# Performance work log

Measured on AMD Instinct MI355X. Metric: run time of the kernel, lower is better.

The kernel has to match this reference:

```python
import jax, jax.numpy as jnp
import numpy as np

N_NODES = 50000
N_EDGES = 800000
F_IN = 128
HIDDEN = 32
HEADS = 4
F_OUT = 64
NEG_SLOPE = 0.2


def setup_inputs() -> dict:
    key = jax.random.key(0)
    ks = jax.random.split(key, 9)
    x = jax.random.normal(ks[0], (N_NODES, F_IN), dtype=jnp.float32)
    edge_index = jax.random.randint(ks[1], (2, N_EDGES), 0, N_NODES, dtype=jnp.int64)
    edge_weight = jax.random.uniform(ks[2], (N_EDGES,), dtype=jnp.float32)
    # GATConv parameters
    W = jax.random.normal(ks[3], (F_IN, HEADS * HIDDEN), dtype=jnp.float32) * (1.0 / np.sqrt(F_IN))
    a_src = jax.random.normal(ks[4], (HEADS, HIDDEN), dtype=jnp.float32) * 0.1
    a_dst = jax.random.normal(ks[5], (HEADS, HIDDEN), dtype=jnp.float32) * 0.1
    bias = jnp.zeros((HEADS * HIDDEN,), dtype=jnp.float32)
    # output linear
    W2 = jax.random.normal(ks[6], (HEADS * HIDDEN, F_OUT), dtype=jnp.float32) * (1.0 / np.sqrt(HEADS * HIDDEN))
    b2 = jnp.zeros((F_OUT,), dtype=jnp.float32)
    return {"x": x, "edge_index": edge_index, "edge_weight": edge_weight,
            "W": W, "a_src": a_src, "a_dst": a_dst, "bias": bias,
            "W2": W2, "b2": b2}


def reference(x, edge_index, edge_weight, W, a_src, a_dst, bias, W2, b2):
    src, dst = edge_index[0], edge_index[1]
    # linear transform per head: [N, H, C]
    h = (x @ W).reshape(-1, HEADS, HIDDEN)
    # per-node attention logits: [N, H]
    alpha_s = jnp.einsum('nhc,hc->nh', h, a_src)
    alpha_d = jnp.einsum('nhc,hc->nh', h, a_dst)
    # per-edge scores: [E, H]
    e = alpha_s[src] + alpha_d[dst]
    e = jnp.where(e >= 0, e, NEG_SLOPE * e)  # LeakyReLU(0.2)
    # segment softmax over destination neighborhoods
    m = jax.ops.segment_max(e, dst, num_segments=N_NODES)  # [N, H]
    ex = jnp.exp(e - m[dst])
    denom = jax.ops.segment_sum(ex, dst, num_segments=N_NODES)  # [N, H]
    alpha = ex / (denom[dst] + 1e-16)  # [E, H]
    # weighted scatter-add aggregation: [N, H, C]
    msgs = alpha[:, :, None] * h[src]
    out = jax.ops.segment_sum(msgs, dst, num_segments=N_NODES)
    out = out.reshape(-1, HEADS * HIDDEN) + bias
    out = jax.nn.elu(out)
    return out @ W2 + b2
```

## Files before the change

kernel.cpp:

```cpp
#include <hip/hip_runtime.h>

#define N_NODES 50000
#define N_EDGES 800000
#define F_IN 128
#define HH 128
#define HEADS 4
#define HIDDEN 32
#define F_OUT 64
#define NEG_SLOPE 0.2f
#define CAP 64

#define NODE_BLOCKS ((N_NODES + 31) / 32)
#define FILL_BLOCKS ((N_EDGES / 4 + 255) / 256)
#define ZERO_BLOCKS ((N_NODES + 255) / 256)

typedef __attribute__((ext_vector_type(8))) short short8v;
typedef __attribute__((ext_vector_type(4))) float float4v;

__device__ __forceinline__ unsigned short f2bf(float f) {
    unsigned int u = __float_as_uint(f);
    u = (u + 0x7FFFu + ((u >> 16) & 1u)) >> 16;
    return (unsigned short)u;
}
__device__ __forceinline__ float bf2f(unsigned short s) {
    return __uint_as_float((unsigned int)s << 16);
}

__global__ __launch_bounds__(256) void k_prep(
    const float* __restrict__ W, const float* __restrict__ a_src,
    const float* __restrict__ a_dst,
    unsigned short* __restrict__ Wf, unsigned short* __restrict__ Waf,
    int* __restrict__ cursor)
{
    const int b = blockIdx.x;
    const int t = threadIdx.x;

    if (b >= 9) {
        int i = (b - 9) * 256 + t;
        if (i < N_NODES) cursor[i] = 0;
        return;
    }

    if (b < 8) {
        const int ks = b >> 1, nn = b & 1;
        const int w = t >> 6, lane = t & 63, l15 = lane & 15, l4 = lane >> 4;
        const int c  = w * 32 + nn * 16 + l15;
        const int kb = ks * 32 + l4 * 8;
        short8v frag;
        #pragma unroll
        for (int j = 0; j < 8; ++j)
            frag[j] = (short)f2bf(W[(size_t)(kb + j) * HH + c]);
        *(short8v*)&Wf[(size_t)((ks * 2 + nn) * 256 + t) * 8] = frag;
        return;
    }

    __shared__ float Wa[F_IN][8];
    #pragma unroll
    for (int i = 0; i < 4; ++i) {
        int idx = t * 4 + i;
        int k = idx >> 3, col = idx & 7;
        const float* av = (col < 4) ? a_src : a_dst;
        int hd = col & 3;
        float s = 0.f;
        #pragma unroll
        for (int cc = 0; cc < 32; ++cc)
            s = fmaf(W[(size_t)k * HH + hd * 32 + cc], av[hd * 32 + cc], s);
        Wa[k][col] = s;
    }
    __syncthreads();

    if (t < 64) {
        const int l15 = t & 15, l4 = t >> 4;
        #pragma unroll
        for (int ks = 0; ks < 4; ++ks) {
            short8v frag;
            #pragma unroll
            for (int j = 0; j < 8; ++j)
                frag[j] = (l15 < 8) ? (short)f2bf(Wa[ks * 32 + l4 * 8 + j][l15]) : (short)0;
            *(short8v*)&Waf[(size_t)(ks * 64 + t) * 8] = frag;
        }
    }
}

__global__ __launch_bounds__(256) void k_node_fill(
    const float* __restrict__ x,
    const unsigned short* __restrict__ Wf, const unsigned short* __restrict__ Waf,
    unsigned short* __restrict__ h_bf,
    float* __restrict__ as_out, float* __restrict__ ad_out,
    const int* __restrict__ ei, int* __restrict__ cursor, int* __restrict__ bucket)
{
    __shared__ __align__(16) unsigned short xs[32][136];

    if (blockIdx.x >= NODE_BLOCKS) {
        int e0 = ((blockIdx.x - NODE_BLOCKS) * 256 + threadIdx.x) * 4;
        if (e0 < N_EDGES) {
            int4 s4 = *(const int4*)&ei[e0];
            int4 d4 = *(const int4*)&ei[N_EDGES + e0];
            bucket[(size_t)d4.x * CAP + (atomicAdd(&cursor[d4.x], 1) & (CAP - 1))] = s4.x;
            bucket[(size_t)d4.y * CAP + (atomicAdd(&cursor[d4.y], 1) & (CAP - 1))] = s4.y;
            bucket[(size_t)d4.z * CAP + (atomicAdd(&cursor[d4.z], 1) & (CAP - 1))] = s4.z;
            bucket[(size_t)d4.w * CAP + (atomicAdd(&cursor[d4.w], 1) & (CAP - 1))] = s4.w;
        }
        return;
    }

    const int tid  = threadIdx.x;
    const int base = blockIdx.x * 32;

    for (int i = tid; i < 32 * 32; i += 256) {
        int r = i >> 5, c4 = i & 31;
        int n = base + r;
        float4 v = (n < N_NODES) ? *(const float4*)&x[(size_t)n * F_IN + c4 * 4]
                                 : make_float4(0.f, 0.f, 0.f, 0.f);
        ushort4 hv;
        hv.x = f2bf(v.x); hv.y = f2bf(v.y); hv.z = f2bf(v.z); hv.w = f2bf(v.w);
        *(ushort4*)&xs[r][c4 * 4] = hv;
    }
    __syncthreads();

    const int w    = tid >> 6;
    const int lane = tid & 63;
    const int l15  = lane & 15;
    const int l4   = lane >> 4;

    short8v bfrag[4][2], wafrag[4];
    #pragma unroll
    for (int ks = 0; ks < 4; ++ks) {
        bfrag[ks][0] = *(const short8v*)&Wf[(size_t)((ks * 2 + 0) * 256 + tid) * 8];
        bfrag[ks][1] = *(const short8v*)&Wf[(size_t)((ks * 2 + 1) * 256 + tid) * 8];
        wafrag[ks]   = *(const short8v*)&Waf[(size_t)(ks * 64 + lane) * 8];
    }

    float4v acc[2][2] = {};
    float4v accL[2] = {};
    #pragma unroll
    for (int ks = 0; ks < 4; ++ks) {
        short8v a0 = *(const short8v*)&xs[l15][ks * 32 + l4 * 8];
        short8v a1 = *(const short8v*)&xs[16 + l15][ks * 32 + l4 * 8];
        acc[0][0] = __builtin_amdgcn_mfma_f32_16x16x32_bf16(a0, bfrag[ks][0], acc[0][0], 0, 0, 0);
        acc[0][1] = __builtin_amdgcn_mfma_f32_16x16x32_bf16(a0, bfrag[ks][1], acc[0][1], 0, 0, 0);
        acc[1][0] = __builtin_amdgcn_mfma_f32_16x16x32_bf16(a1, bfrag[ks][0], acc[1][0], 0, 0, 0);
        acc[1][1] = __builtin_amdgcn_mfma_f32_16x16x32_bf16(a1, bfrag[ks][1], acc[1][1], 0, 0, 0);
        accL[0]   = __builtin_amdgcn_mfma_f32_16x16x32_bf16(a0, wafrag[ks], accL[0], 0, 0, 0);
        accL[1]   = __builtin_amdgcn_mfma_f32_16x16x32_bf16(a1, wafrag[ks], accL[1], 0, 0, 0);
    }

    if (w == 0 && l15 < 8) {
        #pragma unroll
        for (int m = 0; m < 2; ++m) {
            #pragma unroll
            for (int reg = 0; reg < 4; ++reg) {
                int node = base + m * 16 + l4 * 4 + reg;
                if (node >= N_NODES) continue;
                float lg = accL[m][reg];
                if (l15 < 4) as_out[node * HEADS + l15]       = lg;
                else         ad_out[node * HEADS + (l15 - 4)] = lg;
            }
        }
    }

    __syncthreads();
    #pragma unroll
    for (int m = 0; m < 2; ++m) {
        #pragma unroll
        for (int reg = 0; reg < 4; ++reg) {
            int r = m * 16 + l4 * 4 + reg;
            xs[r][w * 32 + l15]      = f2bf(acc[m][0][reg]);
            xs[r][w * 32 + 16 + l15] = f2bf(acc[m][1][reg]);
        }
    }
    __syncthreads();
    for (int i = tid; i < 32 * 16; i += 256) {
        int r = i >> 4, c8 = i & 15;
        int n = base + r;
        if (n < N_NODES)
            *(short8v*)&h_bf[(size_t)n * HH + c8 * 8] = *(const short8v*)&xs[r][c8 * 8];
    }
}

__global__ __launch_bounds__(256) void k_gather(
    const int* __restrict__ cnt_arr, const int* __restrict__ bucket,
    const float* __restrict__ as_, const float* __restrict__ ad_,
    const unsigned short* __restrict__ h_bf, unsigned short* __restrict__ agg_bf)
{
    int gid = blockIdx.x * 256 + threadIdx.x;
    int n = gid >> 6;
    if (n >= N_NODES) return;
    const int lane = gid & 63;
    const int hd  = lane >> 4;
    const int e16 = lane & 15;

    const float advv = ad_[n * 4 + hd];
    const int cnt = cnt_arr[n];
    const int* brow = &bucket[(size_t)n * CAP];

    float accx = 0.f, accy = 0.f, sum = 0.f;

    for (int cb = 0; cb < cnt; cb += 16) {
        int m = cnt - cb; if (m > 16) m = 16;
        int s = 0; float exown = 0.f;
        if (e16 < m) {
            s = brow[cb + e16];
            float lg = as_[s * 4 + hd] + advv;
            lg = lg >= 0.f ? lg : NEG_SLOPE * lg;
            exown = __expf(lg);
        }

#define GAT_BODY(j)                                                            \
        {                                                                      \
            float al = __shfl(exown, (hd << 4) + (j));                         \
            int   sj = __shfl(s,     (hd << 4) + (j));                         \
            unsigned int hv = *(const unsigned int*)&h_bf[(size_t)sj * HH + lane * 2]; \
            sum += al;                                                         \
            accx = fmaf(al, __uint_as_float((hv & 0xFFFFu) << 16), accx);      \
            accy = fmaf(al, __uint_as_float(hv & 0xFFFF0000u), accy);          \
        }

        if (m == 16) {
            #pragma unroll
            for (int j = 0; j < 16; ++j) GAT_BODY(j)
        } else {
            for (int j = 0; j < m; ++j) GAT_BODY(j)
        }
#undef GAT_BODY
    }

    float inv = 1.f / (sum + 1e-16f);
    unsigned int packed = (unsigned int)f2bf(accx * inv)
                        | ((unsigned int)f2bf(accy * inv) << 16);
    *(unsigned int*)&agg_bf[(size_t)n * HH + lane * 2] = packed;
}

__global__ __launch_bounds__(256) void k_output(
    const unsigned short* __restrict__ agg_bf, const float* __restrict__ bias,
    const float* __restrict__ W2, const float* __restrict__ b2,
    float* __restrict__ out)
{
    __shared__ float eb[64][132];

    const int tid  = threadIdx.x;
    const int base = blockIdx.x * 64;

    for (int i = tid; i < 64 * 16; i += 256) {
        int r = i >> 4, c8 = i & 15;
        int n = base + r;
        float v[8];
        if (n < N_NODES) {
            ushort4 p0 = *(const ushort4*)&agg_bf[(size_t)n * HH + c8 * 8];
            ushort4 p1 = *(const ushort4*)&agg_bf[(size_t)n * HH + c8 * 8 + 4];
            v[0] = bf2f(p0.x); v[1] = bf2f(p0.y); v[2] = bf2f(p0.z); v[3] = bf2f(p0.w);
            v[4] = bf2f(p1.x); v[5] = bf2f(p1.y); v[6] = bf2f(p1.z); v[7] = bf2f(p1.w);
        } else {
            #pragma unroll
            for (int j = 0; j < 8; ++j) v[j] = 0.f;
        }
        #pragma unroll
        for (int j = 0; j < 8; ++j) {
            float t = v[j] + bias[c8 * 8 + j];
            eb[r][c8 * 8 + j] = t > 0.f ? t : __expf(t) - 1.f;
        }
    }
    __syncthreads();

    const int cg = tid & 15;
    const int q  = tid >> 4;

    float4 b2v = *(const float4*)&b2[cg * 4];
    float4 acc[4] = { b2v, b2v, b2v, b2v };
    for (int k4 = 0; k4 < 32; ++k4) {
        const float* wr = &W2[(k4 * 4) * F_OUT + cg * 4];
        float4 w0 = *(const float4*)(wr);
        float4 w1 = *(const float4*)(wr + F_OUT);
        float4 w2 = *(const float4*)(wr + 2 * F_OUT);
        float4 w3 = *(const float4*)(wr + 3 * F_OUT);
        #pragma unroll
        for (int j = 0; j < 4; ++j) {
            float4 xv = *(const float4*)&eb[q * 4 + j][k4 * 4];
            acc[j].x = fmaf(xv.x, w0.x, acc[j].x); acc[j].y = fmaf(xv.x, w0.y, acc[j].y);
            acc[j].z = fmaf(xv.x, w0.z, acc[j].z); acc[j].w = fmaf(xv.x, w0.w, acc[j].w);
            acc[j].x = fmaf(xv.y, w1.x, acc[j].x); acc[j].y = fmaf(xv.y, w1.y, acc[j].y);
            acc[j].z = fmaf(xv.y, w1.z, acc[j].z); acc[j].w = fmaf(xv.y, w1.w, acc[j].w);
            acc[j].x = fmaf(xv.z, w2.x, acc[j].x); acc[j].y = fmaf(xv.z, w2.y, acc[j].y);
            acc[j].z = fmaf(xv.z, w2.z, acc[j].z); acc[j].w = fmaf(xv.z, w2.w, acc[j].w);
            acc[j].x = fmaf(xv.w, w3.x, acc[j].x); acc[j].y = fmaf(xv.w, w3.y, acc[j].y);
            acc[j].z = fmaf(xv.w, w3.z, acc[j].z); acc[j].w = fmaf(xv.w, w3.w, acc[j].w);
        }
    }
    #pragma unroll
    for (int j = 0; j < 4; ++j) {
        int n = base + q * 4 + j;
        if (n < N_NODES)
            *(float4*)&out[(size_t)n * F_OUT + cg * 4] = acc[j];
    }
}

extern "C" void kernel_launch(void* const* d_in, const int* in_sizes, int n_in,
                              void* d_out, int out_size, void* d_ws, size_t ws_size,
                              hipStream_t stream)
{
    const float* x     = (const float*)d_in[0];
    const int*   ei    = (const int*)  d_in[1];
    const float* W     = (const float*)d_in[3];
    const float* a_src = (const float*)d_in[4];
    const float* a_dst = (const float*)d_in[5];
    const float* bias  = (const float*)d_in[6];
    const float* W2    = (const float*)d_in[7];
    const float* b2    = (const float*)d_in[8];
    float* out = (float*)d_out;

    char* ws = (char*)d_ws;
    unsigned short* Wf   = (unsigned short*)ws;
    unsigned short* Waf  = Wf + 8 * 256 * 8;
    unsigned short* h_bf = Waf + 4 * 64 * 8;
    float* as_   = (float*)(h_bf + (size_t)N_NODES * HH);
    float* ad_   = as_ + (size_t)N_NODES * HEADS;
    int*   cursor= (int*)(ad_ + (size_t)N_NODES * HEADS);
    int*   bucket= cursor + N_NODES;
    unsigned short* agg_bf = (unsigned short*)(bucket + (size_t)N_NODES * CAP);

    k_prep<<<9 + ZERO_BLOCKS, 256, 0, stream>>>(W, a_src, a_dst, Wf, Waf, cursor);
    k_node_fill<<<NODE_BLOCKS + FILL_BLOCKS, 256, 0, stream>>>(
        x, Wf, Waf, h_bf, as_, ad_, ei, cursor, bucket);
    k_gather<<<(N_NODES * 64 + 255) / 256, 256, 0, stream>>>(cursor, bucket, as_, ad_, h_bf, agg_bf);
    k_output<<<(N_NODES + 63) / 64, 256, 0, stream>>>(agg_bf, bias, W2, b2, out);
}
```

Baseline: 124.9 us.

## Bin edges per 64-node group and fuse gather with output projection

```diff
diff --git a/kernel.cpp b/kernel.cpp
--- a/kernel.cpp
+++ b/kernel.cpp
@@ -5,14 +5,17 @@
 #define F_IN 128
 #define HH 128
 #define HEADS 4
-#define HIDDEN 32
 #define F_OUT 64
 #define NEG_SLOPE 0.2f
-#define CAP 64
+
+#define NBIN ((N_NODES + 63) / 64)
+#define XC 8
+#define CAPXB 256
+#define NCUR (NBIN * XC)
 
 #define NODE_BLOCKS ((N_NODES + 31) / 32)
 #define FILL_BLOCKS ((N_EDGES / 4 + 255) / 256)
-#define ZERO_BLOCKS ((N_NODES + 255) / 256)
+#define ZERO_BLOCKS ((NCUR + 255) / 256)
 
 typedef __attribute__((ext_vector_type(8))) short short8v;
 typedef __attribute__((ext_vector_type(4))) float float4v;
@@ -21,9 +24,6 @@
     unsigned int u = __float_as_uint(f);
     u = (u + 0x7FFFu + ((u >> 16) & 1u)) >> 16;
     return (unsigned short)u;
-}
-__device__ __forceinline__ float bf2f(unsigned short s) {
-    return __uint_as_float((unsigned int)s << 16);
 }
 
 __global__ __launch_bounds__(256) void k_prep(
@@ -37,7 +37,7 @@
 
     if (b >= 9) {
         int i = (b - 9) * 256 + t;
-        if (i < N_NODES) cursor[i] = 0;
+        if (i < NCUR) cursor[i] = 0;
         return;
     }
 
@@ -87,19 +87,27 @@
     const unsigned short* __restrict__ Wf, const unsigned short* __restrict__ Waf,
     unsigned short* __restrict__ h_bf,
     float* __restrict__ as_out, float* __restrict__ ad_out,
-    const int* __restrict__ ei, int* __restrict__ cursor, int* __restrict__ bucket)
+    const int* __restrict__ ei, int* __restrict__ cursor, unsigned int* __restrict__ bins)
 {
     __shared__ __align__(16) unsigned short xs[32][136];
 
     if (blockIdx.x >= NODE_BLOCKS) {
+        const int vx = blockIdx.x & 7;
         int e0 = ((blockIdx.x - NODE_BLOCKS) * 256 + threadIdx.x) * 4;
         if (e0 < N_EDGES) {
             int4 s4 = *(const int4*)&ei[e0];
             int4 d4 = *(const int4*)&ei[N_EDGES + e0];
-            bucket[(size_t)d4.x * CAP + (atomicAdd(&cursor[d4.x], 1) & (CAP - 1))] = s4.x;
-            bucket[(size_t)d4.y * CAP + (atomicAdd(&cursor[d4.y], 1) & (CAP - 1))] = s4.y;
-            bucket[(size_t)d4.z * CAP + (atomicAdd(&cursor[d4.z], 1) & (CAP - 1))] = s4.z;
-            bucket[(size_t)d4.w * CAP + (atomicAdd(&cursor[d4.w], 1) & (CAP - 1))] = s4.w;
+            #define PUTEDGE(S, D)                                              \
+            {                                                                  \
+                int idx = ((D) >> 6) * XC + vx;                                \
+                int sl = atomicAdd(&cursor[idx], 1);                           \
+                if (sl < CAPXB)                                                \
+                    bins[(size_t)idx * CAPXB + sl] =                           \
+                        ((unsigned int)(S) << 6) | (unsigned int)((D) & 63);   \
+            }
+            PUTEDGE(s4.x, d4.x) PUTEDGE(s4.y, d4.y)
+            PUTEDGE(s4.z, d4.z) PUTEDGE(s4.w, d4.w)
+            #undef PUTEDGE
         }
         return;
     }
@@ -178,95 +186,115 @@
     }
 }
 
-__global__ __launch_bounds__(256) void k_gather(
-    const int* __restrict__ cnt_arr, const int* __restrict__ bucket,
+__global__ __launch_bounds__(256) void k_gather_out(
+    const int* __restrict__ cursor, const unsigned int* __restrict__ bins,
     const float* __restrict__ as_, const float* __restrict__ ad_,
-    const unsigned short* __restrict__ h_bf, unsigned short* __restrict__ agg_bf)
+    const unsigned short* __restrict__ h_bf,
+    const float* __restrict__ bias, const float* __restrict__ W2,
+    const float* __restrict__ b2, float* __restrict__ out)
 {
-    int gid = blockIdx.x * 256 + threadIdx.x;
-    int n = gid >> 6;
-    if (n >= N_NODES) return;
-    const int lane = gid & 63;
-    const int hd  = lane >> 4;
-    const int e16 = lane & 15;
-
-    const float advv = ad_[n * 4 + hd];
-    const int cnt = cnt_arr[n];
-    const int* brow = &bucket[(size_t)n * CAP];
-
-    float accx = 0.f, accy = 0.f, sum = 0.f;
-
-    for (int cb = 0; cb < cnt; cb += 16) {
-        int m = cnt - cb; if (m > 16) m = 16;
-        int s = 0; float exown = 0.f;
-        if (e16 < m) {
-            s = brow[cb + e16];
-            float lg = as_[s * 4 + hd] + advv;
-            lg = lg >= 0.f ? lg : NEG_SLOPE * lg;
-            exown = __expf(lg);
-        }
+    __shared__ unsigned int stg[XC * CAPXB];
+    __shared__ unsigned short srcs[XC * CAPXB];
+    __shared__ int lcnt[64], loff[64], lcur[64];
+    __shared__ int scnt[XC], soff[XC], tot_s;
+    __shared__ float eb[64][132];
+    __shared__ float biasl[HH];
+
+    const int bin = blockIdx.x;
+    const int tid = threadIdx.x;
+
+    if (tid < 64) { lcnt[tid] = 0; lcur[tid] = 0; }
+    if (tid < HH) biasl[tid] = bias[tid];
+    if (tid < XC) {
+        int c = cursor[bin * XC + tid];
+        scnt[tid] = c < CAPXB ? c : CAPXB;
+    }
+    __syncthreads();
+    if (tid == 0) {
+        int r = 0;
+        #pragma unroll
+        for (int j = 0; j < XC; ++j) { soff[j] = r; r += scnt[j]; }
+        tot_s = r;
+    }
+    __syncthreads();
+    #pragma unroll
+    for (int sg = 0; sg < XC; ++sg) {
+        int c = scnt[sg], o = soff[sg];
+        const unsigned int* bp = &bins[(size_t)(bin * XC + sg) * CAPXB];
+        for (int i = tid; i < c; i += 256) {
+            unsigned int u = bp[i];
+            stg[o + i] = u;
+            atomicAdd(&lcnt[u & 63], 1);
+        }
+    }
+    __syncthreads();
+    if (tid == 0) {
+        int r = 0;
+        #pragma unroll
+        for (int j = 0; j < 64; ++j) { loff[j] = r; r += lcnt[j]; }
+    }
+    __syncthreads();
+    const int tot = tot_s;
+    for (int i = tid; i < tot; i += 256) {
+        unsigned int u = stg[i];
+        int d = u & 63;
+        int sl = loff[d] + atomicAdd(&lcur[d], 1);
+        srcs[sl] = (unsigned short)(u >> 6);
+    }
+    __syncthreads();
+
+    const int wv   = tid >> 6;
+    const int lane = tid & 63;
+    const int hd   = lane >> 4;
+    const int e16  = lane & 15;
+
+    for (int i = 0; i < 16; ++i) {
+        int ln = wv * 16 + i;
+        int n = bin * 64 + ln;
+        if (n >= N_NODES) continue;
+        const int deg = lcnt[ln], off = loff[ln];
+        const float advv = ad_[n * 4 + hd];
+
+        float accx = 0.f, accy = 0.f, sum = 0.f;
+        for (int cb = 0; cb < deg; cb += 16) {
+            int m = deg - cb; if (m > 16) m = 16;
+            int s = 0; float exown = 0.f;
+            if (e16 < m) {
+                s = srcs[off + cb + e16];
+                float lg = as_[s * 4 + hd] + advv;
+                lg = lg >= 0.f ? lg : NEG_SLOPE * lg;
+                exown = __expf(lg);
+            }
 
 #define GAT_BODY(j)                                                            \
-        {                                                                      \
-            float al = __shfl(exown, (hd << 4) + (j));                         \
-            int   sj = __shfl(s,     (hd << 4) + (j));                         \
-            unsigned int hv = *(const unsigned int*)&h_bf[(size_t)sj * HH + lane * 2]; \
-            sum += al;                                                         \
-            accx = fmaf(al, __uint_as_float((hv & 0xFFFFu) << 16), accx);      \
-            accy = fmaf(al, __uint_as_float(hv & 0xFFFF0000u), accy);          \
-        }
-
-        if (m == 16) {
-            #pragma unroll
-            for (int j = 0; j < 16; ++j) GAT_BODY(j)
-        } else {
-            for (int j = 0; j < m; ++j) GAT_BODY(j)
-        }
+            {                                                                  \
+                float al = __shfl(exown, (hd << 4) + (j));                     \
+                int   sj = __shfl(s,     (hd << 4) + (j));                     \
+                unsigned int hv = *(const unsigned int*)&h_bf[(size_t)sj * HH + lane * 2]; \
+                sum += al;                                                     \
+                accx = fmaf(al, __uint_as_float((hv & 0xFFFFu) << 16), accx);  \
+                accy = fmaf(al, __uint_as_float(hv & 0xFFFF0000u), accy);      \
+            }
+            if (m == 16) {
+                #pragma unroll
+                for (int j = 0; j < 16; ++j) GAT_BODY(j)
+            } else {
+                for (int j = 0; j < m; ++j) GAT_BODY(j)
+            }
 #undef GAT_BODY
-    }
-
-    float inv = 1.f / (sum + 1e-16f);
-    unsigned int packed = (unsigned int)f2bf(accx * inv)
-                        | ((unsigned int)f2bf(accy * inv) << 16);
-    *(unsigned int*)&agg_bf[(size_t)n * HH + lane * 2] = packed;
-}
-
-__global__ __launch_bounds__(256) void k_output(
-    const unsigned short* __restrict__ agg_bf, const float* __restrict__ bias,
-    const float* __restrict__ W2, const float* __restrict__ b2,
-    float* __restrict__ out)
-{
-    __shared__ float eb[64][132];
-
-    const int tid  = threadIdx.x;
-    const int base = blockIdx.x * 64;
-
-    for (int i = tid; i < 64 * 16; i += 256) {
-        int r = i >> 4, c8 = i & 15;
-        int n = base + r;
-        float v[8];
-        if (n < N_NODES) {
-            ushort4 p0 = *(const ushort4*)&agg_bf[(size_t)n * HH + c8 * 8];
-            ushort4 p1 = *(const ushort4*)&agg_bf[(size_t)n * HH + c8 * 8 + 4];
-            v[0] = bf2f(p0.x); v[1] = bf2f(p0.y); v[2] = bf2f(p0.z); v[3] = bf2f(p0.w);
-            v[4] = bf2f(p1.x); v[5] = bf2f(p1.y); v[6] = bf2f(p1.z); v[7] = bf2f(p1.w);
-        } else {
-            #pragma unroll
-            for (int j = 0; j < 8; ++j) v[j] = 0.f;
-        }
-        #pragma unroll
-        for (int j = 0; j < 8; ++j) {
-            float t = v[j] + bias[c8 * 8 + j];
-            eb[r][c8 * 8 + j] = t > 0.f ? t : __expf(t) - 1.f;
-        }
+        }
+        float inv = 1.f / (sum + 1e-16f);
+        float v0 = accx * inv + biasl[lane * 2];
+        float v1 = accy * inv + biasl[lane * 2 + 1];
+        eb[ln][lane * 2]     = v0 > 0.f ? v0 : __expf(v0) - 1.f;
+        eb[ln][lane * 2 + 1] = v1 > 0.f ? v1 : __expf(v1) - 1.f;
     }
     __syncthreads();
 
     const int cg = tid & 15;
     const int q  = tid >> 4;
-
     float4 b2v = *(const float4*)&b2[cg * 4];
-    float4 acc[4] = { b2v, b2v, b2v, b2v };
+    float4 oacc[4] = { b2v, b2v, b2v, b2v };
     for (int k4 = 0; k4 < 32; ++k4) {
         const float* wr = &W2[(k4 * 4) * F_OUT + cg * 4];
         float4 w0 = *(const float4*)(wr);
@@ -276,21 +304,21 @@
         #pragma unroll
         for (int j = 0; j < 4; ++j) {
             float4 xv = *(const float4*)&eb[q * 4 + j][k4 * 4];
-            acc[j].x = fmaf(xv.x, w0.x, acc[j].x); acc[j].y = fmaf(xv.x, w0.y, acc[j].y);
-            acc[j].z = fmaf(xv.x, w0.z, acc[j].z); acc[j].w = fmaf(xv.x, w0.w, acc[j].w);
-            acc[j].x = fmaf(xv.y, w1.x, acc[j].x); acc[j].y = fmaf(xv.y, w1.y, acc[j].y);
-            acc[j].z = fmaf(xv.y, w1.z, acc[j].z); acc[j].w = fmaf(xv.y, w1.w, acc[j].w);
-            acc[j].x = fmaf(xv.z, w2.x, acc[j].x); acc[j].y = fmaf(xv.z, w2.y, acc[j].y);
-            acc[j].z = fmaf(xv.z, w2.z, acc[j].z); acc[j].w = fmaf(xv.z, w2.w, acc[j].w);
-            acc[j].x = fmaf(xv.w, w3.x, acc[j].x); acc[j].y = fmaf(xv.w, w3.y, acc[j].y);
-            acc[j].z = fmaf(xv.w, w3.z, acc[j].z); acc[j].w = fmaf(xv.w, w3.w, acc[j].w);
+            oacc[j].x = fmaf(xv.x, w0.x, oacc[j].x); oacc[j].y = fmaf(xv.x, w0.y, oacc[j].y);
+            oacc[j].z = fmaf(xv.x, w0.z, oacc[j].z); oacc[j].w = fmaf(xv.x, w0.w, oacc[j].w);
+            oacc[j].x = fmaf(xv.y, w1.x, oacc[j].x); oacc[j].y = fmaf(xv.y, w1.y, oacc[j].y);
+            oacc[j].z = fmaf(xv.y, w1.z, oacc[j].z); oacc[j].w = fmaf(xv.y, w1.w, oacc[j].w);
+            oacc[j].x = fmaf(xv.z, w2.x, oacc[j].x); oacc[j].y = fmaf(xv.z, w2.y, oacc[j].y);
+            oacc[j].z = fmaf(xv.z, w2.z, oacc[j].z); oacc[j].w = fmaf(xv.z, w2.w, oacc[j].w);
+            oacc[j].x = fmaf(xv.w, w3.x, oacc[j].x); oacc[j].y = fmaf(xv.w, w3.y, oacc[j].y);
+            oacc[j].z = fmaf(xv.w, w3.z, oacc[j].z); oacc[j].w = fmaf(xv.w, w3.w, oacc[j].w);
         }
     }
     #pragma unroll
     for (int j = 0; j < 4; ++j) {
-        int n = base + q * 4 + j;
+        int n = bin * 64 + q * 4 + j;
         if (n < N_NODES)
-            *(float4*)&out[(size_t)n * F_OUT + cg * 4] = acc[j];
+            *(float4*)&out[(size_t)n * F_OUT + cg * 4] = oacc[j];
     }
 }
 
@@ -315,12 +343,11 @@
     float* as_   = (float*)(h_bf + (size_t)N_NODES * HH);
     float* ad_   = as_ + (size_t)N_NODES * HEADS;
     int*   cursor= (int*)(ad_ + (size_t)N_NODES * HEADS);
-    int*   bucket= cursor + N_NODES;
-    unsigned short* agg_bf = (unsigned short*)(bucket + (size_t)N_NODES * CAP);
+    unsigned int* bins = (unsigned int*)(cursor + 6400);
 
     k_prep<<<9 + ZERO_BLOCKS, 256, 0, stream>>>(W, a_src, a_dst, Wf, Waf, cursor);
     k_node_fill<<<NODE_BLOCKS + FILL_BLOCKS, 256, 0, stream>>>(
-        x, Wf, Waf, h_bf, as_, ad_, ei, cursor, bucket);
-    k_gather<<<(N_NODES * 64 + 255) / 256, 256, 0, stream>>>(cursor, bucket, as_, ad_, h_bf, agg_bf);
-    k_output<<<(N_NODES + 63) / 64, 256, 0, stream>>>(agg_bf, bias, W2, b2, out);
-}
+        x, Wf, Waf, h_bf, as_, ad_, ei, cursor, bins);
+    k_gather_out<<<NBIN, 256, 0, stream>>>(
+        cursor, bins, as_, ad_, h_bf, bias, W2, b2, out);
+}
```

Measured after the change: 202.8 us. +62.3%, slower.

## Bin edges by 64-node groups then counting-sort into compact CSR

Applied to the files above, without the earlier changes.

```diff
diff --git a/kernel.cpp b/kernel.cpp
--- a/kernel.cpp
+++ b/kernel.cpp
@@ -5,14 +5,18 @@
 #define F_IN 128
 #define HH 128
 #define HEADS 4
-#define HIDDEN 32
 #define F_OUT 64
 #define NEG_SLOPE 0.2f
-#define CAP 64
+
+#define NBIN ((N_NODES + 63) / 64)
+#define XC 8
+#define CAPXB 256
+#define NCUR (NBIN * XC)
+#define BINCAP (XC * CAPXB)
 
 #define NODE_BLOCKS ((N_NODES + 31) / 32)
 #define FILL_BLOCKS ((N_EDGES / 4 + 255) / 256)
-#define ZERO_BLOCKS ((N_NODES + 255) / 256)
+#define ZERO_BLOCKS ((NCUR + 255) / 256)
 
 typedef __attribute__((ext_vector_type(8))) short short8v;
 typedef __attribute__((ext_vector_type(4))) float float4v;
@@ -37,7 +41,7 @@
 
     if (b >= 9) {
         int i = (b - 9) * 256 + t;
-        if (i < N_NODES) cursor[i] = 0;
+        if (i < NCUR) cursor[i] = 0;
         return;
     }
 
@@ -87,19 +91,27 @@
     const unsigned short* __restrict__ Wf, const unsigned short* __restrict__ Waf,
     unsigned short* __restrict__ h_bf,
     float* __restrict__ as_out, float* __restrict__ ad_out,
-    const int* __restrict__ ei, int* __restrict__ cursor, int* __restrict__ bucket)
+    const int* __restrict__ ei, int* __restrict__ cursor, unsigned int* __restrict__ bins)
 {
     __shared__ __align__(16) unsigned short xs[32][136];
 
     if (blockIdx.x >= NODE_BLOCKS) {
+        const int vx = blockIdx.x & 7;
         int e0 = ((blockIdx.x - NODE_BLOCKS) * 256 + threadIdx.x) * 4;
         if (e0 < N_EDGES) {
             int4 s4 = *(const int4*)&ei[e0];
             int4 d4 = *(const int4*)&ei[N_EDGES + e0];
-            bucket[(size_t)d4.x * CAP + (atomicAdd(&cursor[d4.x], 1) & (CAP - 1))] = s4.x;
-            bucket[(size_t)d4.y * CAP + (atomicAdd(&cursor[d4.y], 1) & (CAP - 1))] = s4.y;
-            bucket[(size_t)d4.z * CAP + (atomicAdd(&cursor[d4.z], 1) & (CAP - 1))] = s4.z;
-            bucket[(size_t)d4.w * CAP + (atomicAdd(&cursor[d4.w], 1) & (CAP - 1))] = s4.w;
+            #define PUTEDGE(S, D)                                              \
+            {                                                                  \
+                int idx = ((D) >> 6) * XC + vx;                                \
+                int sl = atomicAdd(&cursor[idx], 1);                           \
+                if (sl < CAPXB)                                                \
+                    bins[(size_t)idx * CAPXB + sl] =                           \
+                        ((unsigned int)(S) << 6) | (unsigned int)((D) & 63);   \
+            }
+            PUTEDGE(s4.x, d4.x) PUTEDGE(s4.y, d4.y)
+            PUTEDGE(s4.z, d4.z) PUTEDGE(s4.w, d4.w)
+            #undef PUTEDGE
         }
         return;
     }
@@ -178,8 +190,63 @@
     }
 }
 
+__global__ __launch_bounds__(256) void k_sort(
+    const int* __restrict__ cursor, const unsigned int* __restrict__ bins,
+    unsigned short* __restrict__ srcs_g, int2* __restrict__ offdeg)
+{
+    __shared__ unsigned int stg[BINCAP];
+    __shared__ int lcnt[64], loff[64], lcur[64];
+    __shared__ int scnt[XC], soff[XC], tot_s;
+
+    const int bin = blockIdx.x;
+    const int tid = threadIdx.x;
+
+    if (tid < 64) { lcnt[tid] = 0; lcur[tid] = 0; }
+    if (tid < XC) {
+        int c = cursor[bin * XC + tid];
+        scnt[tid] = c < CAPXB ? c : CAPXB;
+    }
+    __syncthreads();
+    if (tid == 0) {
+        int r = 0;
+        #pragma unroll
+        for (int j = 0; j < XC; ++j) { soff[j] = r; r += scnt[j]; }
+        tot_s = r;
+    }
+    __syncthreads();
+    #pragma unroll
+    for (int sg = 0; sg < XC; ++sg) {
+        int c = scnt[sg], o = soff[sg];
+        const unsigned int* bp = &bins[(size_t)(bin * XC + sg) * CAPXB];
+        for (int i = tid; i < c; i += 256) {
+            unsigned int u = bp[i];
+            stg[o + i] = u;
+            atomicAdd(&lcnt[u & 63], 1);
+        }
+    }
+    __syncthreads();
+    if (tid == 0) {
+        int r = 0;
+        #pragma unroll
+        for (int j = 0; j < 64; ++j) { loff[j] = r; r += lcnt[j]; }
+    }
+    __syncthreads();
+    const int tot = tot_s;
+    for (int i = tid; i < tot; i += 256) {
+        unsigned int u = stg[i];
+        int d = u & 63;
+        int sl = loff[d] + atomicAdd(&lcur[d], 1);
+        srcs_g[(size_t)bin * BINCAP + sl] = (unsigned short)(u >> 6);
+    }
+    if (tid < 64) {
+        int n = bin * 64 + tid;
+        if (n < N_NODES)
+            offdeg[n] = make_int2(bin * BINCAP + loff[tid], lcnt[tid]);
+    }
+}
+
 __global__ __launch_bounds__(256) void k_gather(
-    const int* __restrict__ cnt_arr, const int* __restrict__ bucket,
+    const int2* __restrict__ offdeg, const unsigned short* __restrict__ srcs_g,
     const float* __restrict__ as_, const float* __restrict__ ad_,
     const unsigned short* __restrict__ h_bf, unsigned short* __restrict__ agg_bf)
 {
@@ -191,13 +258,14 @@
     const int e16 = lane & 15;
 
     const float advv = ad_[n * 4 + hd];
-    const int cnt = cnt_arr[n];
-    const int* brow = &bucket[(size_t)n * CAP];
+    const int2 od = offdeg[n];
+    const unsigned short* brow = &srcs_g[od.x];
+    const int deg = od.y;
 
     float accx = 0.f, accy = 0.f, sum = 0.f;
 
-    for (int cb = 0; cb < cnt; cb += 16) {
-        int m = cnt - cb; if (m > 16) m = 16;
+    for (int cb = 0; cb < deg; cb += 16) {
+        int m = deg - cb; if (m > 16) m = 16;
         int s = 0; float exown = 0.f;
         if (e16 < m) {
             s = brow[cb + e16];
@@ -315,12 +383,16 @@
     float* as_   = (float*)(h_bf + (size_t)N_NODES * HH);
     float* ad_   = as_ + (size_t)N_NODES * HEADS;
     int*   cursor= (int*)(ad_ + (size_t)N_NODES * HEADS);
-    int*   bucket= cursor + N_NODES;
-    unsigned short* agg_bf = (unsigned short*)(bucket + (size_t)N_NODES * CAP);
+    unsigned int* bins = (unsigned int*)(cursor + 6400);
+    unsigned short* srcs_g = (unsigned short*)(bins + (size_t)NBIN * BINCAP);
+    int2*  offdeg = (int2*)(srcs_g + (size_t)NBIN * BINCAP);
+    unsigned short* agg_bf = (unsigned short*)(offdeg + N_NODES + 2);
 
     k_prep<<<9 + ZERO_BLOCKS, 256, 0, stream>>>(W, a_src, a_dst, Wf, Waf, cursor);
     k_node_fill<<<NODE_BLOCKS + FILL_BLOCKS, 256, 0, stream>>>(
-        x, Wf, Waf, h_bf, as_, ad_, ei, cursor, bucket);
-    k_gather<<<(N_NODES * 64 + 255) / 256, 256, 0, stream>>>(cursor, bucket, as_, ad_, h_bf, agg_bf);
+        x, Wf, Waf, h_bf, as_, ad_, ei, cursor, bins);
+    k_sort<<<NBIN, 256, 0, stream>>>(cursor, bins, srcs_g, offdeg);
+    k_gather<<<(N_NODES * 64 + 255) / 256, 256, 0, stream>>>(
+        offdeg, srcs_g, as_, ad_, h_bf, agg_bf);
     k_output<<<(N_NODES + 63) / 64, 256, 0, stream>>>(agg_bf, bias, W2, b2, out);
 }
```

Measured after the change: 132.3 us. 5.9% more time.

## Store neighbor lists as 16-bit indices and interleave fill with node blocks

Applied to the files above, without the earlier changes.

```diff
diff --git a/kernel.cpp b/kernel.cpp
--- a/kernel.cpp
+++ b/kernel.cpp
@@ -5,13 +5,13 @@
 #define F_IN 128
 #define HH 128
 #define HEADS 4
-#define HIDDEN 32
 #define F_OUT 64
 #define NEG_SLOPE 0.2f
 #define CAP 64
 
 #define NODE_BLOCKS ((N_NODES + 31) / 32)
-#define FILL_BLOCKS ((N_EDGES / 4 + 255) / 256)
+#define FILLB (N_EDGES / 256)
+#define TOTAL_BLOCKS (NODE_BLOCKS + FILLB)
 #define ZERO_BLOCKS ((N_NODES + 255) / 256)
 
 typedef __attribute__((ext_vector_type(8))) short short8v;
@@ -87,25 +87,30 @@
     const unsigned short* __restrict__ Wf, const unsigned short* __restrict__ Waf,
     unsigned short* __restrict__ h_bf,
     float* __restrict__ as_out, float* __restrict__ ad_out,
-    const int* __restrict__ ei, int* __restrict__ cursor, int* __restrict__ bucket)
+    const int* __restrict__ ei, int* __restrict__ cursor,
+    unsigned short* __restrict__ srcs_g)
 {
     __shared__ __align__(16) unsigned short xs[32][136];
 
-    if (blockIdx.x >= NODE_BLOCKS) {
-        int e0 = ((blockIdx.x - NODE_BLOCKS) * 256 + threadIdx.x) * 4;
-        if (e0 < N_EDGES) {
-            int4 s4 = *(const int4*)&ei[e0];
-            int4 d4 = *(const int4*)&ei[N_EDGES + e0];
-            bucket[(size_t)d4.x * CAP + (atomicAdd(&cursor[d4.x], 1) & (CAP - 1))] = s4.x;
-            bucket[(size_t)d4.y * CAP + (atomicAdd(&cursor[d4.y], 1) & (CAP - 1))] = s4.y;
-            bucket[(size_t)d4.z * CAP + (atomicAdd(&cursor[d4.z], 1) & (CAP - 1))] = s4.z;
-            bucket[(size_t)d4.w * CAP + (atomicAdd(&cursor[d4.w], 1) & (CAP - 1))] = s4.w;
+    const int g = blockIdx.x;
+    if (g % 3 != 0) {
+        const int fidx = g - g / 3 - 1;
+        if (fidx < FILLB) {
+            int e = fidx * 256 + threadIdx.x;
+            int S = ei[e];
+            int D = ei[N_EDGES + e];
+            int sl = atomicAdd(&cursor[D], 1) & (CAP - 1);
+            srcs_g[(size_t)D * CAP + sl] = (unsigned short)S;
         }
         return;
     }
 
     const int tid  = threadIdx.x;
-    const int base = blockIdx.x * 32;
+    const int base = (g / 3) * 32;
+    const int w    = tid >> 6;
+    const int lane = tid & 63;
+    const int l15  = lane & 15;
+    const int l4   = lane >> 4;
 
     for (int i = tid; i < 32 * 32; i += 256) {
         int r = i >> 5, c4 = i & 31;
@@ -117,11 +122,6 @@
         *(ushort4*)&xs[r][c4 * 4] = hv;
     }
     __syncthreads();
-
-    const int w    = tid >> 6;
-    const int lane = tid & 63;
-    const int l15  = lane & 15;
-    const int l4   = lane >> 4;
 
     short8v bfrag[4][2], wafrag[4];
     #pragma unroll
@@ -179,7 +179,7 @@
 }
 
 __global__ __launch_bounds__(256) void k_gather(
-    const int* __restrict__ cnt_arr, const int* __restrict__ bucket,
+    const int* __restrict__ cursor, const unsigned short* __restrict__ srcs_g,
     const float* __restrict__ as_, const float* __restrict__ ad_,
     const unsigned short* __restrict__ h_bf, unsigned short* __restrict__ agg_bf)
 {
@@ -191,13 +191,13 @@
     const int e16 = lane & 15;
 
     const float advv = ad_[n * 4 + hd];
-    const int cnt = cnt_arr[n];
-    const int* brow = &bucket[(size_t)n * CAP];
+    int deg = cursor[n]; if (deg > CAP) deg = CAP;
+    const unsigned short* brow = &srcs_g[(size_t)n * CAP];
 
     float accx = 0.f, accy = 0.f, sum = 0.f;
 
-    for (int cb = 0; cb < cnt; cb += 16) {
-        int m = cnt - cb; if (m > 16) m = 16;
+    for (int cb = 0; cb < deg; cb += 16) {
+        int m = deg - cb; if (m > 16) m = 16;
         int s = 0; float exown = 0.f;
         if (e16 < m) {
             s = brow[cb + e16];
@@ -315,12 +315,13 @@
     float* as_   = (float*)(h_bf + (size_t)N_NODES * HH);
     float* ad_   = as_ + (size_t)N_NODES * HEADS;
     int*   cursor= (int*)(ad_ + (size_t)N_NODES * HEADS);
-    int*   bucket= cursor + N_NODES;
-    unsigned short* agg_bf = (unsigned short*)(bucket + (size_t)N_NODES * CAP);
+    unsigned short* srcs_g = (unsigned short*)(cursor + N_NODES);
+    unsigned short* agg_bf = srcs_g + (size_t)N_NODES * CAP;
 
     k_prep<<<9 + ZERO_BLOCKS, 256, 0, stream>>>(W, a_src, a_dst, Wf, Waf, cursor);
-    k_node_fill<<<NODE_BLOCKS + FILL_BLOCKS, 256, 0, stream>>>(
-        x, Wf, Waf, h_bf, as_, ad_, ei, cursor, bucket);
-    k_gather<<<(N_NODES * 64 + 255) / 256, 256, 0, stream>>>(cursor, bucket, as_, ad_, h_bf, agg_bf);
+    k_node_fill<<<TOTAL_BLOCKS, 256, 0, stream>>>(
+        x, Wf, Waf, h_bf, as_, ad_, ei, cursor, srcs_g);
+    k_gather<<<(N_NODES * 64 + 255) / 256, 256, 0, stream>>>(
+        cursor, srcs_g, as_, ad_, h_bf, agg_bf);
     k_output<<<(N_NODES + 63) / 64, 256, 0, stream>>>(agg_bf, bias, W2, b2, out);
 }
```

Measured after the change: 120.7 us. -3.4%, faster.
